# Performance work log

Hardware: AMD Instinct MI355X
Metric: run time of the kernel (lower is better)

Reference implementation:

```python
import jax, jax.numpy as jnp
import numpy as np

B, C, N, K, D = 4, 64, 40960, 16, 128
EPS = 1e-5  # BatchNorm2d default eps


def _bn_relu(x, g, b, m, v):
    # inference BN over channel axis 1, then ReLU (pt_utils.Conv2d default activation)
    scale = g / jnp.sqrt(v + EPS)
    shift = b - m * scale
    return jax.nn.relu(x * scale[None, :, None, None] + shift[None, :, None, None])


def setup_inputs() -> dict:
    key = jax.random.key(0)
    ks = jax.random.split(key, 16)
    feature = jax.random.normal(ks[0], (B, C, N, 1), jnp.float32)
    neigh_idx = jax.random.randint(ks[1], (B, N, K), 0, N)
    w1 = jax.random.normal(ks[2], (C, C), jnp.float32) * 0.05
    w2 = jax.random.normal(ks[3], (D, C), jnp.float32) * 0.05
    w3 = jax.random.normal(ks[4], (D, C), jnp.float32) * 0.05
    def bn(kg, km, kv, n):
        g = 1.0 + 0.1 * jax.random.normal(kg, (n,), jnp.float32)
        b = 0.1 * jax.random.normal(km, (n,), jnp.float32)
        m = 0.1 * jax.random.normal(kv, (n,), jnp.float32)
        v = jax.random.uniform(jax.random.fold_in(kv, 1), (n,), jnp.float32, 0.5, 1.5)
        return g, b, m, v
    g1, b1, m1, v1 = bn(ks[5], ks[6], ks[7], C)
    g2, b2, m2, v2 = bn(ks[8], ks[9], ks[10], D)
    g3, b3, m3, v3 = bn(ks[11], ks[12], ks[13], D)
    return dict(feature=feature, neigh_idx=neigh_idx,
                w1=w1, g1=g1, b1=b1, m1=m1, v1=v1,
                w2=w2, g2=g2, b2=b2, m2=m2, v2=v2,
                w3=w3, g3=g3, b3=b3, m3=m3, v3=v3)


def reference(feature, neigh_idx, w1, g1, b1, m1, v1, w2, g2, b2, m2, v2,
              w3, g3, b3, m3, v3):
    # gather_neighbour: feature [B,C,N,1], neigh_idx [B,N,K] -> [B,C,N,K]
    f = feature[:, :, :, 0]                                   # [B,C,N]
    f_neigh = jax.vmap(lambda fb, ib: fb[:, ib])(f, neigh_idx)  # [B,C,N,K]
    # mlp1: 1x1 conv + BN + ReLU
    h = jnp.einsum('oc,bcnk->bonk', w1, f_neigh)
    h = _bn_relu(h, g1, b1, m1, v1)
    # sum over neighbors
    h = jnp.sum(h, axis=-1, keepdims=True)                    # [B,C,N,1]
    # mlp2
    h = jnp.einsum('oc,bcnk->bonk', w2, h)
    h = _bn_relu(h, g2, b2, m2, v2)
    # mlp3 on original feature (residual branch)
    s = jnp.einsum('oc,bcnk->bonk', w3, feature)
    s = _bn_relu(s, g3, b3, m3, v3)
    return h + s                                              # [B,D,N,1]
```

## Files before the change

### kernel.cpp

```cpp
#include <hip/hip_runtime.h>

#define EPSV 1e-5f
constexpr int Bb = 4, Cc = 64, Nn = 40960, Kk = 16, Dd = 128;
constexpr int G = 4;
constexpr int TPB = Nn / 16;

typedef float f32x4 __attribute__((ext_vector_type(4)));
typedef __bf16 bf16x8 __attribute__((ext_vector_type(8)));
typedef unsigned short us8 __attribute__((ext_vector_type(8)));
typedef unsigned short us4 __attribute__((ext_vector_type(4)));

__device__ inline unsigned short f2bf(float x) {
    unsigned u = __builtin_bit_cast(unsigned, x);
    u += 0x7FFFu + ((u >> 16) & 1u);
    return (unsigned short)(u >> 16);
}

__global__ __launch_bounds__(256) void prep_weights(
    const float* __restrict__ w1, const float* __restrict__ g1, const float* __restrict__ b1,
    const float* __restrict__ m1, const float* __restrict__ v1,
    const float* __restrict__ w2, const float* __restrict__ g2, const float* __restrict__ b2,
    const float* __restrict__ m2, const float* __restrict__ v2,
    const float* __restrict__ w3, const float* __restrict__ g3, const float* __restrict__ b3,
    const float* __restrict__ m3, const float* __restrict__ v3,
    unsigned short* __restrict__ w1s, unsigned short* __restrict__ w2s, unsigned short* __restrict__ w3s,
    float* __restrict__ sh1, float* __restrict__ sh2, float* __restrict__ sh3) {
    const int e = blockIdx.x * 256 + threadIdx.x;
    if (e < 4096) {
        const int o = e >> 6;
        const float sc = g1[o] * rsqrtf(v1[o] + EPSV);
        w1s[e] = f2bf(w1[e] * sc);
    } else if (e < 12288) {
        const int i = e - 4096, o = i >> 6;
        const float sc = g2[o] * rsqrtf(v2[o] + EPSV);
        w2s[i] = f2bf(w2[i] * sc);
    } else if (e < 20480) {
        const int i = e - 12288, o = i >> 6;
        const float sc = g3[o] * rsqrtf(v3[o] + EPSV);
        w3s[i] = f2bf(w3[i] * sc);
    }
    if (e < 64) sh1[e] = b1[e] - m1[e] * (g1[e] * rsqrtf(v1[e] + EPSV));
    else if (e < 192) { const int d = e - 64;  sh2[d] = b2[d] - m2[d] * (g2[d] * rsqrtf(v2[d] + EPSV)); }
    else if (e < 320) { const int d = e - 192; sh3[d] = b3[d] - m3[d] * (g3[d] * rsqrtf(v3[d] + EPSV)); }
}

__global__ __launch_bounds__(256) void passA(const float* __restrict__ f,
                                             const unsigned short* __restrict__ w1s,
                                             const float* __restrict__ sh1,
                                             unsigned short* __restrict__ G1) {
    __shared__ float s[64 * 65];
    __shared__ __attribute__((aligned(16))) unsigned short sg1[64 * 72];

    const int tid = threadIdx.x, w = tid >> 6, lane = tid & 63;
    const int c15 = lane & 15, q = lane >> 4;
    const int b = blockIdx.x / 640;
    const int n0 = (blockIdx.x % 640) * 64;

    const float* src = f + ((size_t)b * Cc + w * 16) * Nn + n0 + lane;
#pragma unroll
    for (int i = 0; i < 16; ++i) s[(w * 16 + i) * 65 + lane] = src[(size_t)i * Nn];

    const int o1 = w * 16 + c15;
    const float sh1v = sh1[o1];
    bf16x8 bw1[2];
#pragma unroll
    for (int ks = 0; ks < 2; ++ks)
        bw1[ks] = __builtin_bit_cast(bf16x8, *(const uint4*)(w1s + o1 * 64 + ks * 32 + q * 8));
    __syncthreads();

#pragma unroll
    for (int mt = 0; mt < 4; ++mt) {
        const int pt = mt * 16 + c15;
        us8 A0, A1;
#pragma unroll
        for (int j = 0; j < 8; ++j) A0[j] = f2bf(s[(q * 8 + j) * 65 + pt]);
#pragma unroll
        for (int j = 0; j < 8; ++j) A1[j] = f2bf(s[(32 + q * 8 + j) * 65 + pt]);
        f32x4 g = {0.f, 0.f, 0.f, 0.f};
        g = __builtin_amdgcn_mfma_f32_16x16x32_bf16(__builtin_bit_cast(bf16x8, A0), bw1[0], g, 0, 0, 0);
        g = __builtin_amdgcn_mfma_f32_16x16x32_bf16(__builtin_bit_cast(bf16x8, A1), bw1[1], g, 0, 0, 0);
#pragma unroll
        for (int r = 0; r < 4; ++r)
            sg1[(mt * 16 + q * 4 + r) * 72 + o1] = f2bf(fmaxf(g[r] + sh1v, 0.f));
    }
    __syncthreads();

    {
        const int p = tid >> 2, ck = tid & 3;
        const uint4 v0 = *(const uint4*)(sg1 + p * 72 + ck * 16);
        const uint4 v1 = *(const uint4*)(sg1 + p * 72 + ck * 16 + 8);
        unsigned short* dst = G1 + ((size_t)b * Nn + n0 + p) * 64 + ck * 16;
        *(uint4*)dst = v0;
        *(uint4*)(dst + 8) = v1;
    }
}

__global__ __launch_bounds__(256, 4) void passB(
    const unsigned short* __restrict__ G1, const float* __restrict__ f,
    const int* __restrict__ idx,
    const unsigned short* __restrict__ w2s, const unsigned short* __restrict__ w3s,
    const float* __restrict__ sh2, const float* __restrict__ sh3,
    float* __restrict__ out) {
    __shared__ __attribute__((aligned(16))) unsigned short s_h1[16 * 72];
    __shared__ float s_out[32 * 133];

    const int tid  = threadIdx.x;
    const int wave = tid >> 6;
    const int lane = tid & 63;
    const int c15  = lane & 15;
    const int q    = lane >> 4;
    const int pg   = tid >> 4;
    const int cg   = tid & 15;

    const int t0  = blockIdx.x * G;
    const int b   = t0 / TPB;
    const int nb0 = (t0 - b * TPB) * 16;

    float sh2v[2], sh3v[2];
    bf16x8 bw2[2][2], bw3[2][2];
#pragma unroll
    for (int nt = 0; nt < 2; ++nt) {
        const int d = wave * 32 + nt * 16 + c15;
        sh2v[nt] = sh2[d];
        sh3v[nt] = sh3[d];
#pragma unroll
        for (int ks = 0; ks < 2; ++ks) {
            bw2[nt][ks] = __builtin_bit_cast(bf16x8, *(const uint4*)(w2s + d * 64 + ks * 32 + q * 8));
            bw3[nt][ks] = __builtin_bit_cast(bf16x8, *(const uint4*)(w3s + d * 64 + ks * 32 + q * 8));
        }
    }

    const unsigned short* G1b = G1 + (size_t)b * Nn * 64;
    const float* fb0 = f + (size_t)b * Cc * Nn;
    const int* idxp = idx + ((size_t)b * Nn + nb0) * Kk;

    int myidx = idxp[tid];

    for (int g = 0; g < G; ++g) {
        const int n0 = nb0 + g * 16;

        const int myidxN = (g + 1 < G) ? idxp[(g + 1) * 256 + tid] : 0;

        const float* fown = fb0 + n0 + c15;
        us8 F0, F1;
#pragma unroll
        for (int j = 0; j < 8; ++j) F0[j] = f2bf(fown[(size_t)(q * 8 + j) * Nn]);
#pragma unroll
        for (int j = 0; j < 8; ++j) F1[j] = f2bf(fown[(size_t)(32 + q * 8 + j) * Nn]);

        float a0 = 0.f, a1 = 0.f, a2 = 0.f, a3 = 0.f;
#pragma unroll
        for (int k = 0; k < 16; ++k) {
            const int nb = __shfl(myidx, (pg & 3) * 16 + k, 64);
            const uint2 d2 = *(const uint2*)(G1b + (size_t)nb * 64 + cg * 4);
            a0 += __builtin_bit_cast(float, d2.x << 16);
            a1 += __builtin_bit_cast(float, d2.x & 0xffff0000u);
            a2 += __builtin_bit_cast(float, d2.y << 16);
            a3 += __builtin_bit_cast(float, d2.y & 0xffff0000u);
        }
        myidx = myidxN;

        __syncthreads();
        us4 hv;
        hv[0] = f2bf(a0); hv[1] = f2bf(a1); hv[2] = f2bf(a2); hv[3] = f2bf(a3);
        *(us4*)(s_h1 + pg * 72 + cg * 4) = hv;
        __syncthreads();

        const unsigned short* h1row = s_h1 + c15 * 72;
        const bf16x8 ah0 = __builtin_bit_cast(bf16x8, *(const uint4*)(h1row + q * 8));
        const bf16x8 ah1 = __builtin_bit_cast(bf16x8, *(const uint4*)(h1row + 32 + q * 8));
        const bf16x8 af0 = __builtin_bit_cast(bf16x8, F0);
        const bf16x8 af1 = __builtin_bit_cast(bf16x8, F1);

        const int prow = (g & 1) * 16;
#pragma unroll
        for (int nt = 0; nt < 2; ++nt) {
            f32x4 h2 = {sh2v[nt], sh2v[nt], sh2v[nt], sh2v[nt]};
            f32x4 s3 = {sh3v[nt], sh3v[nt], sh3v[nt], sh3v[nt]};
            h2 = __builtin_amdgcn_mfma_f32_16x16x32_bf16(ah0, bw2[nt][0], h2, 0, 0, 0);
            h2 = __builtin_amdgcn_mfma_f32_16x16x32_bf16(ah1, bw2[nt][1], h2, 0, 0, 0);
            s3 = __builtin_amdgcn_mfma_f32_16x16x32_bf16(af0, bw3[nt][0], s3, 0, 0, 0);
            s3 = __builtin_amdgcn_mfma_f32_16x16x32_bf16(af1, bw3[nt][1], s3, 0, 0, 0);
            const int d = wave * 32 + nt * 16 + c15;
#pragma unroll
            for (int r = 0; r < 4; ++r)
                s_out[(prow + q * 4 + r) * 133 + d] = fmaxf(h2[r], 0.f) + fmaxf(s3[r], 0.f);
        }
        __syncthreads();

        if (g & 1) {
            const int np = n0 - 16;
            const int dd = tid >> 3;
            const int ck = tid & 7;
#pragma unroll
            for (int r4 = 0; r4 < 4; ++r4) {
                const int d = r4 * 32 + dd;
                f32x4 v;
#pragma unroll
                for (int i = 0; i < 4; ++i) v[i] = s_out[(ck * 4 + i) * 133 + d];
                __builtin_nontemporal_store(v, (f32x4*)(out + ((size_t)b * Dd + d) * Nn + np + ck * 4));
            }
        }
    }
}

extern "C" void kernel_launch(void* const* d_in, const int* in_sizes, int n_in,
                              void* d_out, int out_size, void* d_ws, size_t ws_size,
                              hipStream_t stream) {
    const float* feature = (const float*)d_in[0];
    const int*   neigh   = (const int*)d_in[1];
    const float* w1 = (const float*)d_in[2];
    const float* g1 = (const float*)d_in[3];
    const float* b1 = (const float*)d_in[4];
    const float* m1 = (const float*)d_in[5];
    const float* v1 = (const float*)d_in[6];
    const float* w2 = (const float*)d_in[7];
    const float* g2 = (const float*)d_in[8];
    const float* b2 = (const float*)d_in[9];
    const float* m2 = (const float*)d_in[10];
    const float* v2 = (const float*)d_in[11];
    const float* w3 = (const float*)d_in[12];
    const float* g3 = (const float*)d_in[13];
    const float* b3 = (const float*)d_in[14];
    const float* m3 = (const float*)d_in[15];
    const float* v3 = (const float*)d_in[16];
    float* out = (float*)d_out;

    char* ws = (char*)d_ws;
    unsigned short* G1  = (unsigned short*)ws;
    unsigned short* w1s = (unsigned short*)(ws + 20971520);
    unsigned short* w2s = (unsigned short*)(ws + 20971520 + 8192);
    unsigned short* w3s = (unsigned short*)(ws + 20971520 + 24576);
    float* sh1 = (float*)(ws + 20971520 + 40960);
    float* sh2 = (float*)(ws + 20971520 + 41216);
    float* sh3 = (float*)(ws + 20971520 + 41728);

    prep_weights<<<80, 256, 0, stream>>>(w1, g1, b1, m1, v1, w2, g2, b2, m2, v2,
                                         w3, g3, b3, m3, v3, w1s, w2s, w3s, sh1, sh2, sh3);
    passA<<<Bb * 640, 256, 0, stream>>>(feature, w1s, sh1, G1);
    passB<<<(Bb * TPB) / G, 256, 0, stream>>>(G1, feature, neigh, w2s, w3s,
                                              sh2, sh3, out);
}
```

Measured before the change: 214.4 us.

## Split gather table into channel halves with XCD-pinned gather kernels

Splits the per-point mlp1 output table into two 32-channel halves. A separate gather kernel reduces neighbours for each half and writes the summed h1 to a workspace buffer, then a new kernel runs the mlp2/mlp3 MFMAs from that buffer. Block ids are mapped so that each batch stays on a fixed pair of XCDs, which keeps each half-table (about 2.6MB per batch) resident in the local L2 during the random gathers. The cost is an extra round trip of h1 through global memory and two more kernel launches. If the workspace is too small, the code falls back to a fused kernel that reads from the split layout.

```diff
diff --git a/kernel.cpp b/kernel.cpp
--- a/kernel.cpp
+++ b/kernel.cpp
@@ -4,6 +4,8 @@
 constexpr int Bb = 4, Cc = 64, Nn = 40960, Kk = 16, Dd = 128;
 constexpr int G = 4;
 constexpr int TPB = Nn / 16;
+constexpr int GB_BPB = 640;
+constexpr int GB_NG = Nn / (16 * GB_BPB);
 
 typedef float f32x4 __attribute__((ext_vector_type(4)));
 typedef __bf16 bf16x8 __attribute__((ext_vector_type(8)));
@@ -47,7 +49,8 @@
 __global__ __launch_bounds__(256) void passA(const float* __restrict__ f,
                                              const unsigned short* __restrict__ w1s,
                                              const float* __restrict__ sh1,
-                                             unsigned short* __restrict__ G1) {
+                                             unsigned short* __restrict__ G1a,
+                                             unsigned short* __restrict__ G1b) {
     __shared__ float s[64 * 65];
     __shared__ __attribute__((aligned(16))) unsigned short sg1[64 * 72];
 
@@ -89,15 +92,144 @@
         const int p = tid >> 2, ck = tid & 3;
         const uint4 v0 = *(const uint4*)(sg1 + p * 72 + ck * 16);
         const uint4 v1 = *(const uint4*)(sg1 + p * 72 + ck * 16 + 8);
-        unsigned short* dst = G1 + ((size_t)b * Nn + n0 + p) * 64 + ck * 16;
+        unsigned short* half = (ck < 2) ? G1a : G1b;
+        unsigned short* dst = half + ((size_t)b * Nn + n0 + p) * 32 + (ck & 1) * 16;
         *(uint4*)dst = v0;
         *(uint4*)(dst + 8) = v1;
     }
 }
 
-__global__ __launch_bounds__(256, 4) void passB(
-    const unsigned short* __restrict__ G1, const float* __restrict__ f,
+__global__ __launch_bounds__(256) void gatherH(
+    const unsigned short* __restrict__ G1h,
     const int* __restrict__ idx,
+    unsigned short* __restrict__ h1,
+    const int hofs) {
+    const int tid = threadIdx.x;
+    const int pg = tid >> 4, cg = tid & 15;
+    const int rg = cg >> 3, chg = cg & 7;
+    const int bid = blockIdx.x;
+    const int xcd = bid & 7;
+    const int b = xcd >> 1;
+    const int j = ((bid >> 3) << 1) | (xcd & 1);
+
+    const unsigned short* Gb = G1h + (size_t)b * Nn * 32;
+    unsigned short* h1b = h1 + (size_t)b * Nn * 64 + hofs;
+    const int* idxb = idx + (size_t)b * Nn * Kk;
+
+#pragma unroll
+    for (int it = 0; it < GB_NG; ++it) {
+        const int n0 = (j * GB_NG + it) * 16;
+        const int myidx = __builtin_nontemporal_load(idxb + (size_t)n0 * Kk + tid);
+        float a0 = 0.f, a1 = 0.f, a2 = 0.f, a3 = 0.f;
+#pragma unroll
+        for (int kk = 0; kk < 8; ++kk) {
+            const int nb = __shfl(myidx, (pg & 3) * 16 + kk * 2 + rg, 64);
+            const uint2 d2 = *(const uint2*)(Gb + (size_t)nb * 32 + chg * 4);
+            a0 += __builtin_bit_cast(float, d2.x << 16);
+            a1 += __builtin_bit_cast(float, d2.x & 0xffff0000u);
+            a2 += __builtin_bit_cast(float, d2.y << 16);
+            a3 += __builtin_bit_cast(float, d2.y & 0xffff0000u);
+        }
+        a0 += __shfl_xor(a0, 8, 64);
+        a1 += __shfl_xor(a1, 8, 64);
+        a2 += __shfl_xor(a2, 8, 64);
+        a3 += __shfl_xor(a3, 8, 64);
+        if (rg == 0) {
+            const unsigned lo = (unsigned)f2bf(a0) | ((unsigned)f2bf(a1) << 16);
+            const unsigned hi = (unsigned)f2bf(a2) | ((unsigned)f2bf(a3) << 16);
+            const unsigned long long v = (unsigned long long)lo | ((unsigned long long)hi << 32);
+            __builtin_nontemporal_store(v,
+                (unsigned long long*)(h1b + (size_t)(n0 + pg) * 64 + chg * 4));
+        }
+    }
+}
+
+__global__ __launch_bounds__(256, 4) void passC(
+    const unsigned short* __restrict__ h1, const float* __restrict__ f,
+    const unsigned short* __restrict__ w2s, const unsigned short* __restrict__ w3s,
+    const float* __restrict__ sh2, const float* __restrict__ sh3,
+    float* __restrict__ out) {
+    __shared__ float s_out[32 * 133];
+
+    const int tid  = threadIdx.x;
+    const int wave = tid >> 6;
+    const int lane = tid & 63;
+    const int c15  = lane & 15;
+    const int q    = lane >> 4;
+
+    const int t0  = blockIdx.x * G;
+    const int b   = t0 / TPB;
+    const int nb0 = (t0 - b * TPB) * 16;
+
+    float sh2v[2], sh3v[2];
+    bf16x8 bw2[2][2], bw3[2][2];
+#pragma unroll
+    for (int nt = 0; nt < 2; ++nt) {
+        const int d = wave * 32 + nt * 16 + c15;
+        sh2v[nt] = sh2[d];
+        sh3v[nt] = sh3[d];
+#pragma unroll
+        for (int ks = 0; ks < 2; ++ks) {
+            bw2[nt][ks] = __builtin_bit_cast(bf16x8, *(const uint4*)(w2s + d * 64 + ks * 32 + q * 8));
+            bw3[nt][ks] = __builtin_bit_cast(bf16x8, *(const uint4*)(w3s + d * 64 + ks * 32 + q * 8));
+        }
+    }
+
+    const float* fb0 = f + (size_t)b * Cc * Nn;
+    const unsigned short* h1b = h1 + (size_t)b * Nn * 64;
+
+    for (int g = 0; g < G; ++g) {
+        const int n0 = nb0 + g * 16;
+
+        const float* fown = fb0 + n0 + c15;
+        us8 F0, F1;
+#pragma unroll
+        for (int jj = 0; jj < 8; ++jj) F0[jj] = f2bf(fown[(size_t)(q * 8 + jj) * Nn]);
+#pragma unroll
+        for (int jj = 0; jj < 8; ++jj) F1[jj] = f2bf(fown[(size_t)(32 + q * 8 + jj) * Nn]);
+
+        const unsigned short* h1row = h1b + (size_t)(n0 + c15) * 64;
+        const bf16x8 ah0 = __builtin_bit_cast(bf16x8, *(const uint4*)(h1row + q * 8));
+        const bf16x8 ah1 = __builtin_bit_cast(bf16x8, *(const uint4*)(h1row + 32 + q * 8));
+        const bf16x8 af0 = __builtin_bit_cast(bf16x8, F0);
+        const bf16x8 af1 = __builtin_bit_cast(bf16x8, F1);
+
+        const int prow = (g & 1) * 16;
+#pragma unroll
+        for (int nt = 0; nt < 2; ++nt) {
+            f32x4 h2 = {sh2v[nt], sh2v[nt], sh2v[nt], sh2v[nt]};
+            f32x4 s3 = {sh3v[nt], sh3v[nt], sh3v[nt], sh3v[nt]};
+            h2 = __builtin_amdgcn_mfma_f32_16x16x32_bf16(ah0, bw2[nt][0], h2, 0, 0, 0);
+            h2 = __builtin_amdgcn_mfma_f32_16x16x32_bf16(ah1, bw2[nt][1], h2, 0, 0, 0);
+            s3 = __builtin_amdgcn_mfma_f32_16x16x32_bf16(af0, bw3[nt][0], s3, 0, 0, 0);
+            s3 = __builtin_amdgcn_mfma_f32_16x16x32_bf16(af1, bw3[nt][1], s3, 0, 0, 0);
+            const int d = wave * 32 + nt * 16 + c15;
+#pragma unroll
+            for (int r = 0; r < 4; ++r)
+                s_out[(prow + q * 4 + r) * 133 + d] = fmaxf(h2[r], 0.f) + fmaxf(s3[r], 0.f);
+        }
+
+        if (g & 1) {
+            __syncthreads();
+            const int np = n0 - 16;
+            const int dd = tid >> 3;
+            const int ck = tid & 7;
+#pragma unroll
+            for (int r4 = 0; r4 < 4; ++r4) {
+                const int d = r4 * 32 + dd;
+                f32x4 v;
+#pragma unroll
+                for (int i = 0; i < 4; ++i) v[i] = s_out[(ck * 4 + i) * 133 + d];
+                __builtin_nontemporal_store(v, (f32x4*)(out + ((size_t)b * Dd + d) * Nn + np + ck * 4));
+            }
+            __syncthreads();
+        }
+    }
+}
+
+__global__ __launch_bounds__(256, 4) void passB_fused(
+    const unsigned short* __restrict__ G1a, const unsigned short* __restrict__ G1b,
+    const float* __restrict__ f, const int* __restrict__ idx,
     const unsigned short* __restrict__ w2s, const unsigned short* __restrict__ w3s,
     const float* __restrict__ sh2, const float* __restrict__ sh3,
     float* __restrict__ out) {
@@ -130,7 +262,10 @@
         }
     }
 
-    const unsigned short* G1b = G1 + (size_t)b * Nn * 64;
+    const unsigned short* Gha = G1a + (size_t)b * Nn * 32;
+    const unsigned short* Ghb = G1b + (size_t)b * Nn * 32;
+    const unsigned short* Gh  = (cg < 8) ? Gha : Ghb;
+    const int cgo = (cg & 7) * 4;
     const float* fb0 = f + (size_t)b * Cc * Nn;
     const int* idxp = idx + ((size_t)b * Nn + nb0) * Kk;
 
@@ -138,21 +273,20 @@
 
     for (int g = 0; g < G; ++g) {
         const int n0 = nb0 + g * 16;
-
         const int myidxN = (g + 1 < G) ? idxp[(g + 1) * 256 + tid] : 0;
 
         const float* fown = fb0 + n0 + c15;
         us8 F0, F1;
 #pragma unroll
-        for (int j = 0; j < 8; ++j) F0[j] = f2bf(fown[(size_t)(q * 8 + j) * Nn]);
-#pragma unroll
-        for (int j = 0; j < 8; ++j) F1[j] = f2bf(fown[(size_t)(32 + q * 8 + j) * Nn]);
+        for (int jj = 0; jj < 8; ++jj) F0[jj] = f2bf(fown[(size_t)(q * 8 + jj) * Nn]);
+#pragma unroll
+        for (int jj = 0; jj < 8; ++jj) F1[jj] = f2bf(fown[(size_t)(32 + q * 8 + jj) * Nn]);
 
         float a0 = 0.f, a1 = 0.f, a2 = 0.f, a3 = 0.f;
 #pragma unroll
         for (int k = 0; k < 16; ++k) {
             const int nb = __shfl(myidx, (pg & 3) * 16 + k, 64);
-            const uint2 d2 = *(const uint2*)(G1b + (size_t)nb * 64 + cg * 4);
+            const uint2 d2 = *(const uint2*)(Gh + (size_t)nb * 32 + cgo);
             a0 += __builtin_bit_cast(float, d2.x << 16);
             a1 += __builtin_bit_cast(float, d2.x & 0xffff0000u);
             a2 += __builtin_bit_cast(float, d2.y << 16);
@@ -226,18 +360,34 @@
     const float* v3 = (const float*)d_in[16];
     float* out = (float*)d_out;
 
+    const size_t SZ_HALF = (size_t)Bb * Nn * 32 * 2;
+    const size_t SZ_H1   = (size_t)Bb * Nn * 64 * 2;
+    const size_t SZ_W    = 42240;
+
     char* ws = (char*)d_ws;
-    unsigned short* G1  = (unsigned short*)ws;
-    unsigned short* w1s = (unsigned short*)(ws + 20971520);
-    unsigned short* w2s = (unsigned short*)(ws + 20971520 + 8192);
-    unsigned short* w3s = (unsigned short*)(ws + 20971520 + 24576);
-    float* sh1 = (float*)(ws + 20971520 + 40960);
-    float* sh2 = (float*)(ws + 20971520 + 41216);
-    float* sh3 = (float*)(ws + 20971520 + 41728);
+    unsigned short* G1a = (unsigned short*)ws;
+    unsigned short* G1b = (unsigned short*)(ws + SZ_HALF);
+    const bool split = ws_size >= 2 * SZ_HALF + SZ_H1 + SZ_W;
+    unsigned short* h1 = (unsigned short*)(ws + 2 * SZ_HALF);
+    char* wbase = ws + (split ? 2 * SZ_HALF + SZ_H1 : 2 * SZ_HALF);
+
+    unsigned short* w1s = (unsigned short*)wbase;
+    unsigned short* w2s = (unsigned short*)(wbase + 8192);
+    unsigned short* w3s = (unsigned short*)(wbase + 24576);
+    float* sh1 = (float*)(wbase + 40960);
+    float* sh2 = (float*)(wbase + 41216);
+    float* sh3 = (float*)(wbase + 41728);
 
     prep_weights<<<80, 256, 0, stream>>>(w1, g1, b1, m1, v1, w2, g2, b2, m2, v2,
                                          w3, g3, b3, m3, v3, w1s, w2s, w3s, sh1, sh2, sh3);
-    passA<<<Bb * 640, 256, 0, stream>>>(feature, w1s, sh1, G1);
-    passB<<<(Bb * TPB) / G, 256, 0, stream>>>(G1, feature, neigh, w2s, w3s,
-                                              sh2, sh3, out);
-}
+    passA<<<Bb * 640, 256, 0, stream>>>(feature, w1s, sh1, G1a, G1b);
+    if (split) {
+        const int ggrid = 8 * (GB_BPB / 2);
+        gatherH<<<ggrid, 256, 0, stream>>>(G1a, neigh, h1, 0);
+        gatherH<<<ggrid, 256, 0, stream>>>(G1b, neigh, h1, 32);
+        passC<<<(Bb * TPB) / G, 256, 0, stream>>>(h1, feature, w2s, w3s, sh2, sh3, out);
+    } else {
+        passB_fused<<<(Bb * TPB) / G, 256, 0, stream>>>(G1a, G1b, feature, neigh,
+                                                        w2s, w3s, sh2, sh3, out);
+    }
+}
```

Measured after the change: 265.4 us. 23.8% more time.

## Stash bf16 transposed features in passA and remap passB blocks per XCD

Applied to the files above, without the earlier changes.

passA now also writes the point-major bf16 copy of the input features it already converts, so passB loads two 16-byte vectors per lane instead of 16 strided fp32 loads plus conversions. passB block indices are also remapped so that each XCD (blockIdx & 7) handles a contiguous half of one batch, aiming to keep that batch's G1 gather table local to one XCD's L2. The cost is an extra 20 MB workspace write in passA and a larger workspace.

```diff
diff --git a/kernel.cpp b/kernel.cpp
--- a/kernel.cpp
+++ b/kernel.cpp
@@ -47,7 +47,8 @@
 __global__ __launch_bounds__(256) void passA(const float* __restrict__ f,
                                              const unsigned short* __restrict__ w1s,
                                              const float* __restrict__ sh1,
-                                             unsigned short* __restrict__ G1) {
+                                             unsigned short* __restrict__ G1,
+                                             unsigned short* __restrict__ f_t) {
     __shared__ float s[64 * 65];
     __shared__ __attribute__((aligned(16))) unsigned short sg1[64 * 72];
 
@@ -76,6 +77,13 @@
         for (int j = 0; j < 8; ++j) A0[j] = f2bf(s[(q * 8 + j) * 65 + pt]);
 #pragma unroll
         for (int j = 0; j < 8; ++j) A1[j] = f2bf(s[(32 + q * 8 + j) * 65 + pt]);
+
+        if (mt == w) {
+            unsigned short* dst = f_t + ((size_t)b * Nn + n0 + pt) * 64;
+            *(uint4*)(dst + q * 8)      = __builtin_bit_cast(uint4, A0);
+            *(uint4*)(dst + 32 + q * 8) = __builtin_bit_cast(uint4, A1);
+        }
+
         f32x4 g = {0.f, 0.f, 0.f, 0.f};
         g = __builtin_amdgcn_mfma_f32_16x16x32_bf16(__builtin_bit_cast(bf16x8, A0), bw1[0], g, 0, 0, 0);
         g = __builtin_amdgcn_mfma_f32_16x16x32_bf16(__builtin_bit_cast(bf16x8, A1), bw1[1], g, 0, 0, 0);
@@ -96,7 +104,7 @@
 }
 
 __global__ __launch_bounds__(256, 4) void passB(
-    const unsigned short* __restrict__ G1, const float* __restrict__ f,
+    const unsigned short* __restrict__ G1, const unsigned short* __restrict__ f_t,
     const int* __restrict__ idx,
     const unsigned short* __restrict__ w2s, const unsigned short* __restrict__ w3s,
     const float* __restrict__ sh2, const float* __restrict__ sh3,
@@ -112,9 +120,10 @@
     const int pg   = tid >> 4;
     const int cg   = tid & 15;
 
-    const int t0  = blockIdx.x * G;
-    const int b   = t0 / TPB;
-    const int nb0 = (t0 - b * TPB) * 16;
+    const int xcd = blockIdx.x & 7;
+    const int jb  = blockIdx.x >> 3;
+    const int b   = xcd >> 1;
+    const int nb0 = (((xcd & 1) * 320) + jb) * (G * 16);
 
     float sh2v[2], sh3v[2];
     bf16x8 bw2[2][2], bw3[2][2];
@@ -131,7 +140,7 @@
     }
 
     const unsigned short* G1b = G1 + (size_t)b * Nn * 64;
-    const float* fb0 = f + (size_t)b * Cc * Nn;
+    const unsigned short* ftb = f_t + (size_t)b * Nn * 64;
     const int* idxp = idx + ((size_t)b * Nn + nb0) * Kk;
 
     int myidx = idxp[tid];
@@ -141,12 +150,9 @@
 
         const int myidxN = (g + 1 < G) ? idxp[(g + 1) * 256 + tid] : 0;
 
-        const float* fown = fb0 + n0 + c15;
-        us8 F0, F1;
-#pragma unroll
-        for (int j = 0; j < 8; ++j) F0[j] = f2bf(fown[(size_t)(q * 8 + j) * Nn]);
-#pragma unroll
-        for (int j = 0; j < 8; ++j) F1[j] = f2bf(fown[(size_t)(32 + q * 8 + j) * Nn]);
+        const unsigned short* ftrow = ftb + (size_t)(n0 + c15) * 64;
+        const bf16x8 af0 = __builtin_bit_cast(bf16x8, *(const uint4*)(ftrow + q * 8));
+        const bf16x8 af1 = __builtin_bit_cast(bf16x8, *(const uint4*)(ftrow + 32 + q * 8));
 
         float a0 = 0.f, a1 = 0.f, a2 = 0.f, a3 = 0.f;
 #pragma unroll
@@ -169,8 +175,6 @@
         const unsigned short* h1row = s_h1 + c15 * 72;
         const bf16x8 ah0 = __builtin_bit_cast(bf16x8, *(const uint4*)(h1row + q * 8));
         const bf16x8 ah1 = __builtin_bit_cast(bf16x8, *(const uint4*)(h1row + 32 + q * 8));
-        const bf16x8 af0 = __builtin_bit_cast(bf16x8, F0);
-        const bf16x8 af1 = __builtin_bit_cast(bf16x8, F1);
 
         const int prow = (g & 1) * 16;
 #pragma unroll
@@ -226,18 +230,24 @@
     const float* v3 = (const float*)d_in[16];
     float* out = (float*)d_out;
 
+    const size_t SZ_G1 = (size_t)Bb * Nn * 64 * 2;
+    const size_t SZ_FT = (size_t)Bb * Nn * 64 * 2;
+
     char* ws = (char*)d_ws;
     unsigned short* G1  = (unsigned short*)ws;
-    unsigned short* w1s = (unsigned short*)(ws + 20971520);
-    unsigned short* w2s = (unsigned short*)(ws + 20971520 + 8192);
-    unsigned short* w3s = (unsigned short*)(ws + 20971520 + 24576);
-    float* sh1 = (float*)(ws + 20971520 + 40960);
-    float* sh2 = (float*)(ws + 20971520 + 41216);
-    float* sh3 = (float*)(ws + 20971520 + 41728);
+    unsigned short* f_t = (unsigned short*)(ws + SZ_G1);
+    char* wbase = ws + SZ_G1 + SZ_FT;
+
+    unsigned short* w1s = (unsigned short*)wbase;
+    unsigned short* w2s = (unsigned short*)(wbase + 8192);
+    unsigned short* w3s = (unsigned short*)(wbase + 24576);
+    float* sh1 = (float*)(wbase + 40960);
+    float* sh2 = (float*)(wbase + 41216);
+    float* sh3 = (float*)(wbase + 41728);
 
     prep_weights<<<80, 256, 0, stream>>>(w1, g1, b1, m1, v1, w2, g2, b2, m2, v2,
                                          w3, g3, b3, m3, v3, w1s, w2s, w3s, sh1, sh2, sh3);
-    passA<<<Bb * 640, 256, 0, stream>>>(feature, w1s, sh1, G1);
-    passB<<<(Bb * TPB) / G, 256, 0, stream>>>(G1, feature, neigh, w2s, w3s,
+    passA<<<Bb * 640, 256, 0, stream>>>(feature, w1s, sh1, G1, f_t);
+    passB<<<(Bb * TPB) / G, 256, 0, stream>>>(G1, f_t, neigh, w2s, w3s,
                                               sh2, sh3, out);
 }
```

Measured after the change: 209.9 us. -2.1%, faster.
